# Optimization experiments

Hardware: AMD Instinct MI355X
Metric: run time of the kernel (lower is better)

The kernel has to match this reference:

```python
import jax, jax.numpy as jnp
import numpy as np

ALPHA = 1.0 / 50.0  # dt / tau with dt=1, tau=50

T, B, I, H = 1024, 64, 128, 512


def setup_inputs() -> dict:
    key = jax.random.key(0)
    k1, k2, k3, k4 = jax.random.split(key, 4)
    x = jax.random.normal(k1, (T, B, I), dtype=jnp.float32)
    # input2h.weight ~ N(0, 0.5^2), shape [H, I]
    W_in = 0.5 * jax.random.normal(k2, (H, I), dtype=jnp.float32)
    # h2h.weight ~ N(0, 1/sqrt(H)^2), shape [H, H]
    W_h = jax.random.normal(k3, (H, H), dtype=jnp.float32) / np.sqrt(H).astype(np.float32)
    # initial_hidden ~ U(-1, 1), shape [1, H]
    h0 = jax.random.uniform(k4, (1, H), dtype=jnp.float32) * 2.0 - 1.0
    return {"x": x, "W_in": W_in, "W_h": W_h, "h0": h0}


def reference(x, W_in, W_h, h0):
    # Precompute input projection for all timesteps in one big GEMM:
    # [T, B, I] @ [I, H] -> [T, B, H]
    x_proj = jnp.einsum('tbi,hi->tbh', x, W_in)
    hidden0 = jnp.broadcast_to(h0, (x.shape[1], h0.shape[1]))  # [B, H]

    def step(hidden, xp_t):
        h_new = jax.nn.sigmoid(xp_t + hidden @ W_h.T)
        h_new = hidden * (1.0 - ALPHA) + h_new * ALPHA
        return h_new, h_new

    hidden_final, output = jax.lax.scan(step, hidden0, x_proj)
    return output, hidden_final
```

## Files before the change

### kernel.cpp

```cpp
#include <hip/hip_runtime.h>

#define T_STEPS 1024
#define BATCH   64
#define IDIM    128
#define HDIM    512
#define ALPHA_F 0.02f
#define NLOG2E  (-1.4426950408889634f)

typedef _Float16 half2_t __attribute__((ext_vector_type(2)));
typedef _Float16 f16x8 __attribute__((ext_vector_type(8)));
typedef float f32x4 __attribute__((ext_vector_type(4)));
typedef unsigned int uint32;

__device__ __forceinline__ uint32 pk2(float a, float b) {
  auto p = __builtin_amdgcn_cvt_pkrtz(a, b);
  return __builtin_bit_cast(uint32, p);
}

__device__ __forceinline__ int dot4i8(uint32 a, uint32 b, int c) {
#if __has_builtin(__builtin_amdgcn_sdot4)
  return __builtin_amdgcn_sdot4((int)a, (int)b, c, false);
#else
  int s = c;
  s += (int)(signed char)(a)        * (int)(signed char)(b);
  s += (int)(signed char)(a >> 8)   * (int)(signed char)(b >> 8);
  s += (int)(signed char)(a >> 16)  * (int)(signed char)(b >> 16);
  s += (int)(signed char)(a >> 24)  * (int)(signed char)(b >> 24);
  return s;
#endif
}

__device__ __forceinline__ uint32 pkq(float v0, float v1, float v2, float v3, float inv) {
  int i0 = __float2int_rn(v0 * inv), i1 = __float2int_rn(v1 * inv);
  int i2 = __float2int_rn(v2 * inv), i3 = __float2int_rn(v3 * inv);
  return (uint32)(i0 & 255) | ((uint32)(i1 & 255) << 8) |
         ((uint32)(i2 & 255) << 16) | ((uint32)(i3 & 255) << 24);
}

__device__ __forceinline__ float fast_rcp(float x) {
#if __has_builtin(__builtin_amdgcn_rcpf)
  return __builtin_amdgcn_rcpf(x);
#else
  return 1.0f / x;
#endif
}

__device__ __forceinline__ int dpp_xor1(int x) {
#if __has_builtin(__builtin_amdgcn_mov_dpp)
  return __builtin_amdgcn_mov_dpp(x, 0xB1, 0xF, 0xF, true);
#else
  return __shfl_xor(x, 1);
#endif
}
__device__ __forceinline__ int dpp_xor2(int x) {
#if __has_builtin(__builtin_amdgcn_mov_dpp)
  return __builtin_amdgcn_mov_dpp(x, 0x4E, 0xF, 0xF, true);
#else
  return __shfl_xor(x, 2);
#endif
}
__device__ __forceinline__ int swz_xor4(int x) {
#if __has_builtin(__builtin_amdgcn_ds_swizzle)
  return __builtin_amdgcn_ds_swizzle(x, 0x101F);
#else
  return __shfl_xor(x, 4);
#endif
}
__device__ __forceinline__ float fxor1(float x) {
  return __builtin_bit_cast(float, dpp_xor1(__builtin_bit_cast(int, x)));
}
__device__ __forceinline__ float fxor2(float x) {
  return __builtin_bit_cast(float, dpp_xor2(__builtin_bit_cast(int, x)));
}
__device__ __forceinline__ float fxor4(float x) {
  return __builtin_bit_cast(float, swz_xor4(__builtin_bit_cast(int, x)));
}

__device__ __forceinline__ f16x8 pk8(float4 lo, float4 hi) {
  uint4 u = make_uint4(pk2(lo.x, lo.y), pk2(lo.z, lo.w),
                       pk2(hi.x, hi.y), pk2(hi.z, hi.w));
  return __builtin_bit_cast(f16x8, u);
}

__global__ __launch_bounds__(256) void ctrnn_proj_mfma(
    const float* __restrict__ x,
    const float* __restrict__ Win,
    float* __restrict__ xp,
    int rows) {
  const int lane = threadIdx.x & 63;
  const int wv   = threadIdx.x >> 6;
  const int r16  = lane & 15;
  const int kg   = lane >> 4;
  const int jbase = blockIdx.y * 256 + wv * 64;

  f16x8 bf[4][4];
#pragma unroll
  for (int jt = 0; jt < 4; ++jt) {
#pragma unroll
    for (int kb = 0; kb < 4; ++kb) {
      const float* wp = Win + (size_t)(jbase + 16 * jt + r16) * IDIM + 32 * kb + 8 * kg;
      float4 lo = *(const float4*)(wp);
      float4 hi = *(const float4*)(wp + 4);
      lo.x *= NLOG2E; lo.y *= NLOG2E; lo.z *= NLOG2E; lo.w *= NLOG2E;
      hi.x *= NLOG2E; hi.y *= NLOG2E; hi.z *= NLOG2E; hi.w *= NLOG2E;
      bf[jt][kb] = pk8(lo, hi);
    }
  }

  const int mtiles = rows >> 4;
  for (int mt = blockIdx.x; mt < mtiles; mt += gridDim.x) {
    const int mbase = mt << 4;
    f16x8 af[4];
#pragma unroll
    for (int kb = 0; kb < 4; ++kb) {
      const float* xr = x + (size_t)(mbase + r16) * IDIM + 32 * kb + 8 * kg;
      float4 lo = *(const float4*)(xr);
      float4 hi = *(const float4*)(xr + 4);
      af[kb] = pk8(lo, hi);
    }
    f32x4 acc0 = {0.f, 0.f, 0.f, 0.f};
    f32x4 acc1 = {0.f, 0.f, 0.f, 0.f};
    f32x4 acc2 = {0.f, 0.f, 0.f, 0.f};
    f32x4 acc3 = {0.f, 0.f, 0.f, 0.f};
#pragma unroll
    for (int kb = 0; kb < 4; ++kb) {
      acc0 = __builtin_amdgcn_mfma_f32_16x16x32_f16(bf[0][kb], af[kb], acc0, 0, 0, 0);
      acc1 = __builtin_amdgcn_mfma_f32_16x16x32_f16(bf[1][kb], af[kb], acc1, 0, 0, 0);
      acc2 = __builtin_amdgcn_mfma_f32_16x16x32_f16(bf[2][kb], af[kb], acc2, 0, 0, 0);
      acc3 = __builtin_amdgcn_mfma_f32_16x16x32_f16(bf[3][kb], af[kb], acc3, 0, 0, 0);
    }
    float* row = xp + (size_t)(mbase + r16) * HDIM + jbase + 4 * kg;
    *(float4*)(row)      = *(float4*)&acc0;
    *(float4*)(row + 16) = *(float4*)&acc1;
    *(float4*)(row + 32) = *(float4*)&acc2;
    *(float4*)(row + 48) = *(float4*)&acc3;
  }
}

__global__ __launch_bounds__(512)
__attribute__((amdgpu_waves_per_eu(2, 2)))
void ctrnn_scan(
    const float* __restrict__ xp,
    const float* __restrict__ Wh,
    const float* __restrict__ h0,
    float* __restrict__ out,
    int t0, int ct) {
  const int b = blockIdx.x;
  const int j = threadIdx.x;
  const int g = j & 7;
  const int o = j >> 3;

  __shared__ __attribute__((aligned(16))) unsigned char hq[2][640];

  float m[8];
#pragma unroll
  for (int i = 0; i < 8; ++i) {
    const float4* wr = (const float4*)(Wh + (size_t)(8 * o + (i ^ g)) * HDIM + 64 * g);
    float mm = 0.f;
#pragma unroll
    for (int c = 0; c < 16; ++c) {
      float4 v = wr[c];
      mm = fmaxf(mm, fmaxf(fmaxf(fabsf(v.x), fabsf(v.y)), fmaxf(fabsf(v.z), fabsf(v.w))));
    }
    m[i] = mm;
  }
  {
    float t[8];
#pragma unroll
    for (int i = 0; i < 8; ++i) t[i] = fmaxf(m[i], fxor1(m[i ^ 1]));
#pragma unroll
    for (int i = 0; i < 8; ++i) m[i] = fmaxf(t[i], fxor2(t[i ^ 2]));
#pragma unroll
    for (int i = 0; i < 8; ++i) t[i] = fmaxf(m[i], fxor4(m[i ^ 4]));
#pragma unroll
    for (int i = 0; i < 8; ++i) m[i] = t[i];
  }

  uint32 w[128];
#pragma unroll
  for (int i = 0; i < 8; ++i) {
    const float rm = m[i];
    const float inv = (rm > 0.f) ? 127.f / rm : 0.f;
    const float4* wr = (const float4*)(Wh + (size_t)(8 * o + (i ^ g)) * HDIM + 64 * g);
#pragma unroll
    for (int c = 0; c < 16; ++c) {
      float4 v = wr[c];
      w[i * 16 + c] = pkq(v.x, v.y, v.z, v.w, inv);
    }
  }
  const float afac = m[0] * (1.f / (127.f * 127.f)) * NLOG2E;

  float h;
  if (t0 == 0) h = h0[j];
  else h = out[((size_t)(t0 - 1) * BATCH + b) * HDIM + j];
  hq[0][j + 16 * (j >> 6)] = (unsigned char)(__float2int_rn(h * 127.f));
  __syncthreads();

  const float* xpp = xp + (size_t)b * HDIM + j;
  float* outp = out + ((size_t)t0 * BATCH + b) * HDIM + j;
  const size_t BH = (size_t)BATCH * HDIM;

  int cur = 0;
#pragma unroll 2
  for (int t = 0; t < ct; ++t) {
    const float xpw = *xpp;

    const uint4* hb = (const uint4*)(&hq[cur][80 * g]);
    int a0 = 0, a1 = 0, a2 = 0, a3 = 0, a4 = 0, a5 = 0, a6 = 0, a7 = 0;
#pragma unroll
    for (int c = 0; c < 4; ++c) {
      const uint4 hv = hb[c];
      a0 = dot4i8(w[0 * 16 + 4 * c + 0], hv.x, a0);
      a0 = dot4i8(w[0 * 16 + 4 * c + 1], hv.y, a0);
      a0 = dot4i8(w[0 * 16 + 4 * c + 2], hv.z, a0);
      a0 = dot4i8(w[0 * 16 + 4 * c + 3], hv.w, a0);
      a1 = dot4i8(w[1 * 16 + 4 * c + 0], hv.x, a1);
      a1 = dot4i8(w[1 * 16 + 4 * c + 1], hv.y, a1);
      a1 = dot4i8(w[1 * 16 + 4 * c + 2], hv.z, a1);
      a1 = dot4i8(w[1 * 16 + 4 * c + 3], hv.w, a1);
      a2 = dot4i8(w[2 * 16 + 4 * c + 0], hv.x, a2);
      a2 = dot4i8(w[2 * 16 + 4 * c + 1], hv.y, a2);
      a2 = dot4i8(w[2 * 16 + 4 * c + 2], hv.z, a2);
      a2 = dot4i8(w[2 * 16 + 4 * c + 3], hv.w, a2);
      a3 = dot4i8(w[3 * 16 + 4 * c + 0], hv.x, a3);
      a3 = dot4i8(w[3 * 16 + 4 * c + 1], hv.y, a3);
      a3 = dot4i8(w[3 * 16 + 4 * c + 2], hv.z, a3);
      a3 = dot4i8(w[3 * 16 + 4 * c + 3], hv.w, a3);
      a4 = dot4i8(w[4 * 16 + 4 * c + 0], hv.x, a4);
      a4 = dot4i8(w[4 * 16 + 4 * c + 1], hv.y, a4);
      a4 = dot4i8(w[4 * 16 + 4 * c + 2], hv.z, a4);
      a4 = dot4i8(w[4 * 16 + 4 * c + 3], hv.w, a4);
      a5 = dot4i8(w[5 * 16 + 4 * c + 0], hv.x, a5);
      a5 = dot4i8(w[5 * 16 + 4 * c + 1], hv.y, a5);
      a5 = dot4i8(w[5 * 16 + 4 * c + 2], hv.z, a5);
      a5 = dot4i8(w[5 * 16 + 4 * c + 3], hv.w, a5);
      a6 = dot4i8(w[6 * 16 + 4 * c + 0], hv.x, a6);
      a6 = dot4i8(w[6 * 16 + 4 * c + 1], hv.y, a6);
      a6 = dot4i8(w[6 * 16 + 4 * c + 2], hv.z, a6);
      a6 = dot4i8(w[6 * 16 + 4 * c + 3], hv.w, a6);
      a7 = dot4i8(w[7 * 16 + 4 * c + 0], hv.x, a7);
      a7 = dot4i8(w[7 * 16 + 4 * c + 1], hv.y, a7);
      a7 = dot4i8(w[7 * 16 + 4 * c + 2], hv.z, a7);
      a7 = dot4i8(w[7 * 16 + 4 * c + 3], hv.w, a7);
    }
    const int q0 = a0 + dpp_xor1(a1);
    const int q1 = a2 + dpp_xor1(a3);
    const int q2 = a4 + dpp_xor1(a5);
    const int q3 = a6 + dpp_xor1(a7);
    const int r0 = q0 + dpp_xor2(q1);
    const int r1 = q2 + dpp_xor2(q3);
    const int res = r0 + swz_xor4(r1);

    const float e = exp2f((float)res * afac + xpw);
    const float s = fast_rcp(1.0f + e);
    h = h * (1.0f - ALPHA_F) + s * ALPHA_F;

    hq[cur ^ 1][j + 16 * (j >> 6)] = (unsigned char)(__float2int_rn(h * 127.f));
    __syncthreads();

    *outp = h;
    cur ^= 1;
    xpp += BH;
    outp += BH;
  }

  if (t0 + ct == T_STEPS) {
    out[(size_t)T_STEPS * BATCH * HDIM + (size_t)b * HDIM + j] = h;
  }
}

extern "C" void kernel_launch(void* const* d_in, const int* in_sizes, int n_in,
                              void* d_out, int out_size, void* d_ws, size_t ws_size,
                              hipStream_t stream) {
  const float* x   = (const float*)d_in[0];
  const float* Win = (const float*)d_in[1];
  const float* Wh  = (const float*)d_in[2];
  const float* h0  = (const float*)d_in[3];
  float* out = (float*)d_out;
  float* xp  = (float*)d_ws;

  const size_t step_bytes = (size_t)BATCH * HDIM * sizeof(float);
  int ct_max = (int)(ws_size / step_bytes);
  if (ct_max < 1) ct_max = 1;
  if (ct_max > T_STEPS) ct_max = T_STEPS;

  for (int t0 = 0; t0 < T_STEPS; t0 += ct_max) {
    const int ct = (T_STEPS - t0 < ct_max) ? (T_STEPS - t0) : ct_max;
    const int rows = ct * BATCH;
    const int mtiles = rows >> 4;
    const int gx = (mtiles < 1024) ? mtiles : 1024;
    hipLaunchKernelGGL(ctrnn_proj_mfma, dim3(gx, 2), dim3(256), 0, stream,
                       x + (size_t)t0 * BATCH * IDIM, Win, xp, rows);
    hipLaunchKernelGGL(ctrnn_scan, dim3(BATCH), dim3(512), 0, stream,
                       xp, Wh, h0, out, t0, ct);
  }
}
```

Before: 856.5 us.

## Replace per-thread sdot4 recurrence with int8 MFMA 16x16x64 in scan kernel

The recurrent matvec in the scan kernel moves from per-thread packed int8 dot4 instructions plus DPP cross-lane reductions to int8 MFMA 16x16x64 instructions. Each wave holds a 64-row slice of the quantized W_h as MFMA A fragments, and the quantized hidden vector is broadcast as the B operand. Per-row scales now go through LDS. Only lanes with r16==0 use the MFMA output column to do the sigmoid, state update and stores. This removes the reduction shuffles and most of the dot-product issue count, but 15/16 of each MFMA's output columns are wasted and the elementwise work is concentrated in a quarter of the lanes.

```diff
diff --git a/kernel.cpp b/kernel.cpp
--- a/kernel.cpp
+++ b/kernel.cpp
@@ -10,24 +10,12 @@
 typedef _Float16 half2_t __attribute__((ext_vector_type(2)));
 typedef _Float16 f16x8 __attribute__((ext_vector_type(8)));
 typedef float f32x4 __attribute__((ext_vector_type(4)));
+typedef int i32x4 __attribute__((ext_vector_type(4)));
 typedef unsigned int uint32;
 
 __device__ __forceinline__ uint32 pk2(float a, float b) {
   auto p = __builtin_amdgcn_cvt_pkrtz(a, b);
   return __builtin_bit_cast(uint32, p);
-}
-
-__device__ __forceinline__ int dot4i8(uint32 a, uint32 b, int c) {
-#if __has_builtin(__builtin_amdgcn_sdot4)
-  return __builtin_amdgcn_sdot4((int)a, (int)b, c, false);
-#else
-  int s = c;
-  s += (int)(signed char)(a)        * (int)(signed char)(b);
-  s += (int)(signed char)(a >> 8)   * (int)(signed char)(b >> 8);
-  s += (int)(signed char)(a >> 16)  * (int)(signed char)(b >> 16);
-  s += (int)(signed char)(a >> 24)  * (int)(signed char)(b >> 24);
-  return s;
-#endif
 }
 
 __device__ __forceinline__ uint32 pkq(float v0, float v1, float v2, float v3, float inv) {
@@ -43,37 +31,6 @@
 #else
   return 1.0f / x;
 #endif
-}
-
-__device__ __forceinline__ int dpp_xor1(int x) {
-#if __has_builtin(__builtin_amdgcn_mov_dpp)
-  return __builtin_amdgcn_mov_dpp(x, 0xB1, 0xF, 0xF, true);
-#else
-  return __shfl_xor(x, 1);
-#endif
-}
-__device__ __forceinline__ int dpp_xor2(int x) {
-#if __has_builtin(__builtin_amdgcn_mov_dpp)
-  return __builtin_amdgcn_mov_dpp(x, 0x4E, 0xF, 0xF, true);
-#else
-  return __shfl_xor(x, 2);
-#endif
-}
-__device__ __forceinline__ int swz_xor4(int x) {
-#if __has_builtin(__builtin_amdgcn_ds_swizzle)
-  return __builtin_amdgcn_ds_swizzle(x, 0x101F);
-#else
-  return __shfl_xor(x, 4);
-#endif
-}
-__device__ __forceinline__ float fxor1(float x) {
-  return __builtin_bit_cast(float, dpp_xor1(__builtin_bit_cast(int, x)));
-}
-__device__ __forceinline__ float fxor2(float x) {
-  return __builtin_bit_cast(float, dpp_xor2(__builtin_bit_cast(int, x)));
-}
-__device__ __forceinline__ float fxor4(float x) {
-  return __builtin_bit_cast(float, swz_xor4(__builtin_bit_cast(int, x)));
 }
 
 __device__ __forceinline__ f16x8 pk8(float4 lo, float4 hi) {
@@ -146,126 +103,134 @@
     float* __restrict__ out,
     int t0, int ct) {
   const int b = blockIdx.x;
-  const int j = threadIdx.x;
-  const int g = j & 7;
-  const int o = j >> 3;
-
-  __shared__ __attribute__((aligned(16))) unsigned char hq[2][640];
-
-  float m[8];
-#pragma unroll
-  for (int i = 0; i < 8; ++i) {
-    const float4* wr = (const float4*)(Wh + (size_t)(8 * o + (i ^ g)) * HDIM + 64 * g);
+  const int tid = threadIdx.x;
+  const int w = tid >> 6;
+  const int lane = tid & 63;
+  const int r16 = lane & 15;
+  const int kg = lane >> 4;
+  const int nw = 64 * w;
+  const bool act = (r16 == 0);
+
+  __shared__ __attribute__((aligned(16))) unsigned char hq[2][512];
+  __shared__ __attribute__((aligned(16))) float rml[512];
+
+  float rmax[4];
+#pragma unroll
+  for (int nt = 0; nt < 4; ++nt) {
+    const float4* wr = (const float4*)(Wh + (size_t)(nw + 16 * nt + r16) * HDIM + 128 * kg);
     float mm = 0.f;
 #pragma unroll
-    for (int c = 0; c < 16; ++c) {
+    for (int c = 0; c < 32; ++c) {
       float4 v = wr[c];
       mm = fmaxf(mm, fmaxf(fmaxf(fabsf(v.x), fabsf(v.y)), fmaxf(fabsf(v.z), fabsf(v.w))));
     }
-    m[i] = mm;
-  }
-  {
-    float t[8];
-#pragma unroll
-    for (int i = 0; i < 8; ++i) t[i] = fmaxf(m[i], fxor1(m[i ^ 1]));
-#pragma unroll
-    for (int i = 0; i < 8; ++i) m[i] = fmaxf(t[i], fxor2(t[i ^ 2]));
-#pragma unroll
-    for (int i = 0; i < 8; ++i) t[i] = fmaxf(m[i], fxor4(m[i ^ 4]));
-#pragma unroll
-    for (int i = 0; i < 8; ++i) m[i] = t[i];
-  }
-
-  uint32 w[128];
-#pragma unroll
-  for (int i = 0; i < 8; ++i) {
-    const float rm = m[i];
-    const float inv = (rm > 0.f) ? 127.f / rm : 0.f;
-    const float4* wr = (const float4*)(Wh + (size_t)(8 * o + (i ^ g)) * HDIM + 64 * g);
-#pragma unroll
-    for (int c = 0; c < 16; ++c) {
-      float4 v = wr[c];
-      w[i * 16 + c] = pkq(v.x, v.y, v.z, v.w, inv);
-    }
-  }
-  const float afac = m[0] * (1.f / (127.f * 127.f)) * NLOG2E;
-
-  float h;
-  if (t0 == 0) h = h0[j];
-  else h = out[((size_t)(t0 - 1) * BATCH + b) * HDIM + j];
-  hq[0][j + 16 * (j >> 6)] = (unsigned char)(__float2int_rn(h * 127.f));
+    mm = fmaxf(mm, __shfl_xor(mm, 16));
+    mm = fmaxf(mm, __shfl_xor(mm, 32));
+    rmax[nt] = mm;
+  }
+  if (kg == 0) {
+#pragma unroll
+    for (int nt = 0; nt < 4; ++nt) rml[nw + 16 * nt + r16] = rmax[nt];
+  }
+
+  i32x4 wf[4][8];
+#pragma unroll
+  for (int nt = 0; nt < 4; ++nt) {
+    const float inv = (rmax[nt] > 0.f) ? 127.f / rmax[nt] : 0.f;
+    const float* rowp = Wh + (size_t)(nw + 16 * nt + r16) * HDIM;
+#pragma unroll
+    for (int ks = 0; ks < 8; ++ks) {
+      const float4* p = (const float4*)(rowp + 64 * ks + 16 * kg);
+      float4 v0 = p[0], v1 = p[1], v2 = p[2], v3 = p[3];
+      i32x4 f;
+      f[0] = (int)pkq(v0.x, v0.y, v0.z, v0.w, inv);
+      f[1] = (int)pkq(v1.x, v1.y, v1.z, v1.w, inv);
+      f[2] = (int)pkq(v2.x, v2.y, v2.z, v2.w, inv);
+      f[3] = (int)pkq(v3.x, v3.y, v3.z, v3.w, inv);
+      wf[nt][ks] = f;
+    }
+  }
   __syncthreads();
 
-  const float* xpp = xp + (size_t)b * HDIM + j;
-  float* outp = out + ((size_t)t0 * BATCH + b) * HDIM + j;
+  float4 afac[4];
+#pragma unroll
+  for (int nt = 0; nt < 4; ++nt) {
+    float4 rv = *(const float4*)&rml[nw + 16 * nt + 4 * kg];
+    const float k = NLOG2E / (127.f * 127.f);
+    afac[nt] = make_float4(rv.x * k, rv.y * k, rv.z * k, rv.w * k);
+  }
+
+  float4 hst[4];
+  if (act) {
+    const float* src = (t0 == 0) ? h0 : (out + ((size_t)(t0 - 1) * BATCH + b) * HDIM);
+#pragma unroll
+    for (int nt = 0; nt < 4; ++nt) {
+      hst[nt] = *(const float4*)(src + nw + 16 * nt + 4 * kg);
+      *((uint32*)&hq[0][nw + 16 * nt + 4 * kg]) =
+          pkq(hst[nt].x, hst[nt].y, hst[nt].z, hst[nt].w, 127.f);
+    }
+  }
+  __syncthreads();
+
+  const float* xpp = xp + (size_t)b * HDIM + nw + 4 * kg;
+  float* outp = out + ((size_t)t0 * BATCH + b) * HDIM + nw + 4 * kg;
   const size_t BH = (size_t)BATCH * HDIM;
 
   int cur = 0;
-#pragma unroll 2
   for (int t = 0; t < ct; ++t) {
-    const float xpw = *xpp;
-
-    const uint4* hb = (const uint4*)(&hq[cur][80 * g]);
-    int a0 = 0, a1 = 0, a2 = 0, a3 = 0, a4 = 0, a5 = 0, a6 = 0, a7 = 0;
-#pragma unroll
-    for (int c = 0; c < 4; ++c) {
-      const uint4 hv = hb[c];
-      a0 = dot4i8(w[0 * 16 + 4 * c + 0], hv.x, a0);
-      a0 = dot4i8(w[0 * 16 + 4 * c + 1], hv.y, a0);
-      a0 = dot4i8(w[0 * 16 + 4 * c + 2], hv.z, a0);
-      a0 = dot4i8(w[0 * 16 + 4 * c + 3], hv.w, a0);
-      a1 = dot4i8(w[1 * 16 + 4 * c + 0], hv.x, a1);
-      a1 = dot4i8(w[1 * 16 + 4 * c + 1], hv.y, a1);
-      a1 = dot4i8(w[1 * 16 + 4 * c + 2], hv.z, a1);
-      a1 = dot4i8(w[1 * 16 + 4 * c + 3], hv.w, a1);
-      a2 = dot4i8(w[2 * 16 + 4 * c + 0], hv.x, a2);
-      a2 = dot4i8(w[2 * 16 + 4 * c + 1], hv.y, a2);
-      a2 = dot4i8(w[2 * 16 + 4 * c + 2], hv.z, a2);
-      a2 = dot4i8(w[2 * 16 + 4 * c + 3], hv.w, a2);
-      a3 = dot4i8(w[3 * 16 + 4 * c + 0], hv.x, a3);
-      a3 = dot4i8(w[3 * 16 + 4 * c + 1], hv.y, a3);
-      a3 = dot4i8(w[3 * 16 + 4 * c + 2], hv.z, a3);
-      a3 = dot4i8(w[3 * 16 + 4 * c + 3], hv.w, a3);
-      a4 = dot4i8(w[4 * 16 + 4 * c + 0], hv.x, a4);
-      a4 = dot4i8(w[4 * 16 + 4 * c + 1], hv.y, a4);
-      a4 = dot4i8(w[4 * 16 + 4 * c + 2], hv.z, a4);
-      a4 = dot4i8(w[4 * 16 + 4 * c + 3], hv.w, a4);
-      a5 = dot4i8(w[5 * 16 + 4 * c + 0], hv.x, a5);
-      a5 = dot4i8(w[5 * 16 + 4 * c + 1], hv.y, a5);
-      a5 = dot4i8(w[5 * 16 + 4 * c + 2], hv.z, a5);
-      a5 = dot4i8(w[5 * 16 + 4 * c + 3], hv.w, a5);
-      a6 = dot4i8(w[6 * 16 + 4 * c + 0], hv.x, a6);
-      a6 = dot4i8(w[6 * 16 + 4 * c + 1], hv.y, a6);
-      a6 = dot4i8(w[6 * 16 + 4 * c + 2], hv.z, a6);
-      a6 = dot4i8(w[6 * 16 + 4 * c + 3], hv.w, a6);
-      a7 = dot4i8(w[7 * 16 + 4 * c + 0], hv.x, a7);
-      a7 = dot4i8(w[7 * 16 + 4 * c + 1], hv.y, a7);
-      a7 = dot4i8(w[7 * 16 + 4 * c + 2], hv.z, a7);
-      a7 = dot4i8(w[7 * 16 + 4 * c + 3], hv.w, a7);
-    }
-    const int q0 = a0 + dpp_xor1(a1);
-    const int q1 = a2 + dpp_xor1(a3);
-    const int q2 = a4 + dpp_xor1(a5);
-    const int q3 = a6 + dpp_xor1(a7);
-    const int r0 = q0 + dpp_xor2(q1);
-    const int r1 = q2 + dpp_xor2(q3);
-    const int res = r0 + swz_xor4(r1);
-
-    const float e = exp2f((float)res * afac + xpw);
-    const float s = fast_rcp(1.0f + e);
-    h = h * (1.0f - ALPHA_F) + s * ALPHA_F;
-
-    hq[cur ^ 1][j + 16 * (j >> 6)] = (unsigned char)(__float2int_rn(h * 127.f));
+    float4 xw[4];
+    if (act) {
+#pragma unroll
+      for (int nt = 0; nt < 4; ++nt) xw[nt] = *(const float4*)(xpp + 16 * nt);
+    }
+
+    i32x4 av[8];
+#pragma unroll
+    for (int ks = 0; ks < 8; ++ks)
+      av[ks] = *(const i32x4*)&hq[cur][64 * ks + 16 * kg];
+
+    i32x4 acc0 = {0, 0, 0, 0};
+    i32x4 acc1 = {0, 0, 0, 0};
+    i32x4 acc2 = {0, 0, 0, 0};
+    i32x4 acc3 = {0, 0, 0, 0};
+#pragma unroll
+    for (int ks = 0; ks < 8; ++ks) {
+      acc0 = __builtin_amdgcn_mfma_i32_16x16x64_i8(wf[0][ks], av[ks], acc0, 0, 0, 0);
+      acc1 = __builtin_amdgcn_mfma_i32_16x16x64_i8(wf[1][ks], av[ks], acc1, 0, 0, 0);
+      acc2 = __builtin_amdgcn_mfma_i32_16x16x64_i8(wf[2][ks], av[ks], acc2, 0, 0, 0);
+      acc3 = __builtin_amdgcn_mfma_i32_16x16x64_i8(wf[3][ks], av[ks], acc3, 0, 0, 0);
+    }
+
+    if (act) {
+#pragma unroll
+      for (int nt = 0; nt < 4; ++nt) {
+        const i32x4 a = (nt == 0) ? acc0 : (nt == 1) ? acc1 : (nt == 2) ? acc2 : acc3;
+        const float4 af = afac[nt];
+        float4 h4 = hst[nt];
+        const float e0 = exp2f((float)a[0] * af.x + xw[nt].x);
+        const float e1 = exp2f((float)a[1] * af.y + xw[nt].y);
+        const float e2 = exp2f((float)a[2] * af.z + xw[nt].z);
+        const float e3 = exp2f((float)a[3] * af.w + xw[nt].w);
+        h4.x = h4.x * (1.0f - ALPHA_F) + fast_rcp(1.0f + e0) * ALPHA_F;
+        h4.y = h4.y * (1.0f - ALPHA_F) + fast_rcp(1.0f + e1) * ALPHA_F;
+        h4.z = h4.z * (1.0f - ALPHA_F) + fast_rcp(1.0f + e2) * ALPHA_F;
+        h4.w = h4.w * (1.0f - ALPHA_F) + fast_rcp(1.0f + e3) * ALPHA_F;
+        hst[nt] = h4;
+        *(float4*)(outp + 16 * nt) = h4;
+        *((uint32*)&hq[cur ^ 1][nw + 16 * nt + 4 * kg]) =
+            pkq(h4.x, h4.y, h4.z, h4.w, 127.f);
+      }
+    }
     __syncthreads();
-
-    *outp = h;
     cur ^= 1;
     xpp += BH;
     outp += BH;
   }
 
-  if (t0 + ct == T_STEPS) {
-    out[(size_t)T_STEPS * BATCH * HDIM + (size_t)b * HDIM + j] = h;
+  if (t0 + ct == T_STEPS && act) {
+    float* fin = out + (size_t)T_STEPS * BATCH * HDIM + (size_t)b * HDIM + nw + 4 * kg;
+#pragma unroll
+    for (int nt = 0; nt < 4; ++nt) *(float4*)(fin + 16 * nt) = hst[nt];
   }
 }
 
```

Result: slower. 1.825 ms (+113.1%).
